# Performance work log

Measured on AMD Instinct MI355X. Metric: run time of the kernel, lower is better.

## Reference

```python
import jax, jax.numpy as jnp
import numpy as np

TOP_K = 4
NORM_TOPK_PROB = True


def _moe_forward(hidden_states, Wr, Wg, Wu, Wd):
    # hidden_states: [B, S, H]; Wr: [E, H]; Wg/Wu: [E, F, H]; Wd: [E, H, F]
    B, S, H = hidden_states.shape
    E = Wr.shape[0]
    x = hidden_states.reshape(-1, H)                     # [T, H]
    T = x.shape[0]

    # Router: softmax in float32 (matches F.softmax(..., dtype=torch.float))
    router_logits = x @ Wr.T                              # [T, E]
    probs = jax.nn.softmax(router_logits.astype(jnp.float32), axis=-1)
    routing_weights, selected_experts = jax.lax.top_k(probs, TOP_K)  # [T, K]
    if NORM_TOPK_PROB:
        routing_weights = routing_weights / jnp.sum(routing_weights, axis=-1, keepdims=True)
    routing_weights = routing_weights.astype(x.dtype)

    # Dense combine matrix: combine[t, e] = routing weight if expert e selected for token t else 0.
    # Equivalent to the sort/gather dispatch + weighted scatter-add in the torch code.
    combine = jnp.zeros((T, E), dtype=x.dtype).at[
        jnp.arange(T)[:, None], selected_experts
    ].add(routing_weights)                               # [T, E]

    # SwiGLU expert MLP: down(silu(gate(x)) * up(x)), evaluated for all experts,
    # then masked/weighted by combine (zero weight == token not routed to expert).
    hg = jnp.einsum('td,efd->tef', x, Wg)                # [T, E, F]
    hu = jnp.einsum('td,efd->tef', x, Wu)                # [T, E, F]
    act = jax.nn.silu(hg) * hu                           # [T, E, F]
    out = jnp.einsum('tef,te,edf->td', act, combine, Wd) # [T, H]
    return out.reshape(B, S, H)


def setup_inputs() -> dict:
    key = jax.random.key(0)
    k0, k1, k2, k3, k4 = jax.random.split(key, 5)
    B, S, H, E, F = 2, 2048, 2048, 16, 768
    scale = 0.02
    return {
        'hidden_states': jax.random.normal(k0, (B, S, H), dtype=jnp.float32),
        'Wr': jax.random.normal(k1, (E, H), dtype=jnp.float32) * scale,
        'Wg': jax.random.normal(k2, (E, F, H), dtype=jnp.float32) * scale,
        'Wu': jax.random.normal(k3, (E, F, H), dtype=jnp.float32) * scale,
        'Wd': jax.random.normal(k4, (E, H, F), dtype=jnp.float32) * scale,
    }


def reference(hidden_states, Wr, Wg, Wu, Wd):
    return _moe_forward(hidden_states, Wr, Wg, Wu, Wd)
```

## Files before the change

kernel.cpp:

```cpp
#include <hip/hip_runtime.h>
#include <hip/hip_bf16.h>

#define H_DIM 2048
#define F_DIM 768
#define E_NUM 16
#define T_TOK 4096
#define TOPK  4
#define TK_ROWS (T_TOK * TOPK)
#define MAX_TILES 160

typedef __attribute__((ext_vector_type(8))) short bf16x8;
typedef __attribute__((ext_vector_type(4))) float f32x4;

static __device__ __forceinline__ float bf2f(unsigned short u) {
    return __uint_as_float(((unsigned)u) << 16);
}
static __device__ __forceinline__ unsigned short f2bu(float f) {
    __hip_bfloat16 h = __float2bfloat16(f);
    return *(unsigned short*)&h;
}

static __device__ __forceinline__ void gl16(const unsigned short* g, unsigned short* l) {
    __builtin_amdgcn_global_load_lds(
        (__attribute__((address_space(1))) void*)(g),
        (__attribute__((address_space(3))) void*)(l),
        16, 0, 0);
}

static __device__ __forceinline__ void stage8(unsigned short* dst, const void* src,
                                              size_t eoff, bool f32) {
    if (f32) {
        const float* s = (const float*)src + eoff;
        float4 a = *(const float4*)s;
        float4 b = *(const float4*)(s + 4);
        __align__(16) unsigned short u[8] = {
            f2bu(a.x), f2bu(a.y), f2bu(a.z), f2bu(a.w),
            f2bu(b.x), f2bu(b.y), f2bu(b.z), f2bu(b.w)};
        *(uint4*)dst = *(const uint4*)u;
    } else {
        *(uint4*)dst = *(const uint4*)((const unsigned short*)src + eoff);
    }
}

__global__ void probe_kernel(const unsigned short* __restrict__ wr, int* __restrict__ flag) {
    const int tid = threadIdx.x;
    int maxe = 0;
    for (int i = tid; i < 512; i += 64) {
        int e = (wr[i] >> 7) & 0xFF;
        maxe = max(maxe, e);
    }
    for (int off = 32; off > 0; off >>= 1)
        maxe = max(maxe, __shfl_down(maxe, off, 64));
    if (tid == 0) flag[0] = (maxe >= 135) ? 1 : 0;
}

__global__ __launch_bounds__(256)
void convert_kernel(unsigned short* __restrict__ dst, const void* __restrict__ src,
                    const int* __restrict__ dflag, size_t n) {
    const size_t i = ((size_t)blockIdx.x * 256 + threadIdx.x) * 8;
    if (i >= n) return;
    stage8(dst + i, src, i, dflag[0] != 0);
}

__global__ __launch_bounds__(256, 2)
void router_kernel(const void* __restrict__ xv,
                   const void* __restrict__ wrv,
                   const int* __restrict__ dflag,
                   float* __restrict__ topk_w,
                   int* __restrict__ topk_e,
                   int* __restrict__ counts) {
    const bool f32 = dflag[0] != 0;
    const int t0 = blockIdx.x * 8;
    __shared__ float xs[8][H_DIM];
    __shared__ float logits_s[8][E_NUM];
    const int tid = threadIdx.x;

    if (f32) {
        const float4* src = (const float4*)((const float*)xv + (size_t)t0 * H_DIM);
        float4* dst = (float4*)&xs[0][0];
        for (int i = tid; i < 8 * H_DIM / 4; i += 256) dst[i] = src[i];
    } else {
        const uint4* src = (const uint4*)((const unsigned short*)xv + (size_t)t0 * H_DIM);
        for (int i = tid; i < 8 * H_DIM / 8; i += 256) {
            uint4 b = src[i];
            const unsigned short* bp = (const unsigned short*)&b;
            float* d = &xs[0][0] + (size_t)i * 8;
#pragma unroll
            for (int j = 0; j < 8; ++j) d[j] = bf2f(bp[j]);
        }
    }
    __syncthreads();

    const int w = tid >> 6;
    const int lane = tid & 63;

    float acc[8][4];
#pragma unroll
    for (int t = 0; t < 8; ++t)
#pragma unroll
        for (int je = 0; je < 4; ++je) acc[t][je] = 0.f;

    for (int i = 0; i < 4; ++i) {
        const int h = i * 512 + lane * 8;
#pragma unroll
        for (int je = 0; je < 4; ++je) {
            const int e = w * 4 + je;
            float wf[8];
            if (f32) {
                const float* wp = (const float*)wrv + (size_t)e * H_DIM + h;
                float4 a = *(const float4*)wp;
                float4 b = *(const float4*)(wp + 4);
                wf[0]=a.x; wf[1]=a.y; wf[2]=a.z; wf[3]=a.w;
                wf[4]=b.x; wf[5]=b.y; wf[6]=b.z; wf[7]=b.w;
            } else {
                uint4 wb = *(const uint4*)((const unsigned short*)wrv + (size_t)e * H_DIM + h);
                const unsigned short* wp = (const unsigned short*)&wb;
#pragma unroll
                for (int j = 0; j < 8; ++j) wf[j] = bf2f(wp[j]);
            }
#pragma unroll
            for (int t = 0; t < 8; ++t) {
                const float* xp = &xs[t][h];
                float s = 0.f;
#pragma unroll
                for (int j = 0; j < 8; ++j) s += xp[j] * wf[j];
                acc[t][je] += s;
            }
        }
    }
#pragma unroll
    for (int t = 0; t < 8; ++t)
#pragma unroll
        for (int je = 0; je < 4; ++je) {
            float v = acc[t][je];
            v += __shfl_down(v, 32, 64); v += __shfl_down(v, 16, 64);
            v += __shfl_down(v, 8, 64);  v += __shfl_down(v, 4, 64);
            v += __shfl_down(v, 2, 64);  v += __shfl_down(v, 1, 64);
            if (lane == 0) logits_s[t][w * 4 + je] = v;
        }
    __syncthreads();

    if (tid < 8) {
        const int t = t0 + tid;
        float l[E_NUM];
#pragma unroll
        for (int i = 0; i < E_NUM; ++i) l[i] = logits_s[tid][i];
        unsigned mask = 0;
        int sel_e[TOPK];
        float sel_v[TOPK];
        for (int k = 0; k < TOPK; ++k) {
            int be = 0; float bv = -1e30f;
            for (int i = 0; i < E_NUM; ++i) {
                if (!(mask & (1u << i)) && l[i] > bv) { bv = l[i]; be = i; }
            }
            mask |= (1u << be);
            sel_e[k] = be; sel_v[k] = bv;
        }
        const float m = sel_v[0];
        float ex[TOPK]; float s = 0.f;
        for (int k = 0; k < TOPK; ++k) { ex[k] = __expf(sel_v[k] - m); s += ex[k]; }
        const float inv = 1.f / s;
        for (int k = 0; k < TOPK; ++k) {
            float wgt = ex[k] * inv;
            if (!f32) wgt = bf2f(f2bu(wgt));
            topk_w[t * TOPK + k] = wgt;
            topk_e[t * TOPK + k] = sel_e[k];
            atomicAdd(&counts[sel_e[k]], 1);
        }
    }
}

__global__ void scan_kernel(const int* __restrict__ counts, int* __restrict__ offsets,
                            int* __restrict__ tiles, int* __restrict__ ntiles) {
    if (threadIdx.x == 0) {
        int s = 0, nt = 0;
        for (int e = 0; e < E_NUM; ++e) {
            offsets[e] = s;
            const int c = counts[e];
            s += c;
            for (int mt = 0; mt * 128 < c && nt < MAX_TILES; ++mt)
                tiles[nt++] = (e << 16) | mt;
        }
        offsets[E_NUM] = s;
        ntiles[0] = nt;
    }
}

__global__ __launch_bounds__(256)
void scatter_kernel(const int* __restrict__ topk_e, const int* __restrict__ offsets,
                    int* __restrict__ cursors, int* __restrict__ row_token) {
    const int i = blockIdx.x * 256 + threadIdx.x;
    if (i < TK_ROWS) {
        const int e = topk_e[i];
        const int pos = offsets[e] + atomicAdd(&cursors[e], 1);
        row_token[pos] = i;
    }
}

__global__ __launch_bounds__(256)
void gateup_fast(const unsigned short* __restrict__ x,
                 const unsigned short* __restrict__ Wg,
                 const unsigned short* __restrict__ Wu,
                 const int* __restrict__ row_token,
                 const int* __restrict__ counts,
                 const int* __restrict__ offsets,
                 const int* __restrict__ tiles,
                 const int* __restrict__ ntiles,
                 __hip_bfloat16* __restrict__ act_buf) {
    const int ti = blockIdx.y;
    if (ti >= ntiles[0]) return;
    const int packed = tiles[ti];
    const int e = packed >> 16, mt = packed & 0xffff;
    const int ft = blockIdx.x;
    const int cnt = counts[e], base = offsets[e];

    __shared__ unsigned short As[128 * 64];
    __shared__ unsigned short Bgs[128 * 64];
    __shared__ unsigned short Bus[128 * 64];
    __shared__ int tok_s[128];

    const int tid = threadIdx.x;
    if (tid < 128) {
        int r = mt * 128 + tid;
        tok_s[tid] = row_token[base + (r < cnt ? r : cnt - 1)] >> 2;
    }
    __syncthreads();

    const int w = tid >> 6;
    const int lane = tid & 63;
    const int subrow = lane >> 3;
    const int sgrp = lane & 7;
    const int lgrp = sgrp ^ subrow;

    const unsigned short* aptr[4];
    const unsigned short* bgptr[4];
    const unsigned short* buptr[4];
    unsigned short* ldsA[4];
    unsigned short* ldsBg[4];
    unsigned short* ldsBu[4];
    const size_t gOff = ((size_t)e * F_DIM + (size_t)ft * 128) * H_DIM;
#pragma unroll
    for (int j = 0; j < 4; ++j) {
        const int r = (w * 4 + j) * 8 + subrow;
        aptr[j]  = x + (size_t)tok_s[r] * H_DIM + lgrp * 8;
        bgptr[j] = Wg + gOff + (size_t)r * H_DIM + lgrp * 8;
        buptr[j] = Wu + gOff + (size_t)r * H_DIM + lgrp * 8;
        const int lo = r * 64 + sgrp * 8;
        ldsA[j]  = &As[lo];
        ldsBg[j] = &Bgs[lo];
        ldsBu[j] = &Bus[lo];
    }

    f32x4 accg[4][4], accu[4][4];
#pragma unroll
    for (int mi = 0; mi < 4; ++mi)
#pragma unroll
        for (int ni = 0; ni < 4; ++ni)
#pragma unroll
            for (int r = 0; r < 4; ++r) { accg[mi][ni][r] = 0.f; accu[mi][ni][r] = 0.f; }

    const int wm = (w >> 1) * 64;
    const int wn = (w & 1) * 64;
    const int lr = lane & 15;
    const int lq = lane >> 4;
    const int gx = lr & 7;
    const int aoff[2] = { (wm + lr) * 64 + ((lq    ) ^ gx) * 8,
                          (wm + lr) * 64 + ((4 + lq) ^ gx) * 8 };
    const int boff[2] = { (wn + lr) * 64 + ((lq    ) ^ gx) * 8,
                          (wn + lr) * 64 + ((4 + lq) ^ gx) * 8 };

    for (int kk = 0; kk < H_DIM / 64; ++kk) {
        const int k0 = kk * 64;
#pragma unroll
        for (int j = 0; j < 4; ++j) {
            gl16(aptr[j] + k0, ldsA[j]);
            gl16(bgptr[j] + k0, ldsBg[j]);
            gl16(buptr[j] + k0, ldsBu[j]);
        }
        __syncthreads();
#pragma unroll
        for (int ks = 0; ks < 2; ++ks) {
            bf16x8 a[4], bg[4], bu[4];
#pragma unroll
            for (int mi = 0; mi < 4; ++mi)
                a[mi] = *(const bf16x8*)&As[aoff[ks] + mi * 1024];
#pragma unroll
            for (int ni = 0; ni < 4; ++ni) {
                bg[ni] = *(const bf16x8*)&Bgs[boff[ks] + ni * 1024];
                bu[ni] = *(const bf16x8*)&Bus[boff[ks] + ni * 1024];
            }
#pragma unroll
            for (int mi = 0; mi < 4; ++mi)
#pragma unroll
                for (int ni = 0; ni < 4; ++ni) {
                    accg[mi][ni] = __builtin_amdgcn_mfma_f32_16x16x32_bf16(a[mi], bg[ni], accg[mi][ni], 0, 0, 0);
                    accu[mi][ni] = __builtin_amdgcn_mfma_f32_16x16x32_bf16(a[mi], bu[ni], accu[mi][ni], 0, 0, 0);
                }
        }
        __syncthreads();
    }

#pragma unroll
    for (int mi = 0; mi < 4; ++mi) {
#pragma unroll
        for (int r = 0; r < 4; ++r) {
            const int row  = wm + mi * 16 + lq * 4 + r;
            const int grow = mt * 128 + row;
            if (grow < cnt) {
                __hip_bfloat16* dst = act_buf + (size_t)(base + grow) * F_DIM + ft * 128 + wn;
#pragma unroll
                for (int ni = 0; ni < 4; ++ni) {
                    const float g = accg[mi][ni][r];
                    const float u = accu[mi][ni][r];
                    const float s = g / (1.f + __expf(-g));
                    dst[ni * 16 + lr] = __float2bfloat16(s * u);
                }
            }
        }
    }
}

__global__ __launch_bounds__(256)
void down_fast(const unsigned short* __restrict__ act,
               const unsigned short* __restrict__ Wd,
               const int* __restrict__ row_token,
               const int* __restrict__ counts,
               const int* __restrict__ offsets,
               const int* __restrict__ tiles,
               const int* __restrict__ ntiles,
               const float* __restrict__ topk_w,
               float* __restrict__ out) {
    const int ti = blockIdx.y;
    if (ti >= ntiles[0]) return;
    const int packed = tiles[ti];
    const int e = packed >> 16, mt = packed & 0xffff;
    const int ht = blockIdx.x;
    const int cnt = counts[e], base = offsets[e];

    __shared__ unsigned short As[128 * 64];
    __shared__ unsigned short Bs[128 * 64];
    __shared__ int tok_s[128];
    __shared__ float w_s[128];

    const int tid = threadIdx.x;
    if (tid < 128) {
        int r = mt * 128 + tid;
        const int t4 = row_token[base + (r < cnt ? r : cnt - 1)];
        tok_s[tid] = t4 >> 2;
        w_s[tid] = topk_w[t4];
    }
    __syncthreads();

    const int w = tid >> 6;
    const int lane = tid & 63;
    const int subrow = lane >> 3;
    const int sgrp = lane & 7;
    const int lgrp = sgrp ^ subrow;

    const unsigned short* aptr[4];
    const unsigned short* bptr[4];
    unsigned short* ldsA[4];
    unsigned short* ldsB[4];
    const size_t hOff = ((size_t)e * H_DIM + (size_t)ht * 128) * F_DIM;
#pragma unroll
    for (int j = 0; j < 4; ++j) {
        const int r = (w * 4 + j) * 8 + subrow;
        int ar = mt * 128 + r;
        ar = (ar < cnt) ? ar : (cnt - 1);
        aptr[j] = act + (size_t)(base + ar) * F_DIM + lgrp * 8;
        bptr[j] = Wd + hOff + (size_t)r * F_DIM + lgrp * 8;
        const int lo = r * 64 + sgrp * 8;
        ldsA[j] = &As[lo];
        ldsB[j] = &Bs[lo];
    }

    f32x4 accd[4][4];
#pragma unroll
    for (int mi = 0; mi < 4; ++mi)
#pragma unroll
        for (int ni = 0; ni < 4; ++ni)
#pragma unroll
            for (int r = 0; r < 4; ++r) accd[mi][ni][r] = 0.f;

    const int wm = (w >> 1) * 64;
    const int wn = (w & 1) * 64;
    const int lr = lane & 15;
    const int lq = lane >> 4;
    const int gx = lr & 7;
    const int aoff[2] = { (wm + lr) * 64 + ((lq    ) ^ gx) * 8,
                          (wm + lr) * 64 + ((4 + lq) ^ gx) * 8 };
    const int boff[2] = { (wn + lr) * 64 + ((lq    ) ^ gx) * 8,
                          (wn + lr) * 64 + ((4 + lq) ^ gx) * 8 };

    for (int kk = 0; kk < F_DIM / 64; ++kk) {
        const int k0 = kk * 64;
#pragma unroll
        for (int j = 0; j < 4; ++j) {
            gl16(aptr[j] + k0, ldsA[j]);
            gl16(bptr[j] + k0, ldsB[j]);
        }
        __syncthreads();
#pragma unroll
        for (int ks = 0; ks < 2; ++ks) {
            bf16x8 a[4], b[4];
#pragma unroll
            for (int mi = 0; mi < 4; ++mi)
                a[mi] = *(const bf16x8*)&As[aoff[ks] + mi * 1024];
#pragma unroll
            for (int ni = 0; ni < 4; ++ni)
                b[ni] = *(const bf16x8*)&Bs[boff[ks] + ni * 1024];
#pragma unroll
            for (int mi = 0; mi < 4; ++mi)
#pragma unroll
                for (int ni = 0; ni < 4; ++ni)
                    accd[mi][ni] = __builtin_amdgcn_mfma_f32_16x16x32_bf16(a[mi], b[ni], accd[mi][ni], 0, 0, 0);
        }
        __syncthreads();
    }

#pragma unroll
    for (int mi = 0; mi < 4; ++mi) {
#pragma unroll
        for (int r = 0; r < 4; ++r) {
            const int row  = wm + mi * 16 + lq * 4 + r;
            const int grow = mt * 128 + row;
            if (grow < cnt) {
                const float wgt = w_s[row];
                float* dst = out + (size_t)tok_s[row] * H_DIM + ht * 128 + wn;
#pragma unroll
                for (int ni = 0; ni < 4; ++ni)
                    atomicAdd(&dst[ni * 16 + lr], accd[mi][ni][r] * wgt);
            }
        }
    }
}

__global__ __launch_bounds__(256, 2)
void gateup_slow(const void* __restrict__ xv, const void* __restrict__ wgv,
                 const void* __restrict__ wuv, const int* __restrict__ dflag,
                 const int* __restrict__ row_token, const int* __restrict__ counts,
                 const int* __restrict__ offsets, __hip_bfloat16* __restrict__ act_buf) {
    const bool f32 = dflag[0] != 0;
    const int e = blockIdx.z, mt = blockIdx.y, ft = blockIdx.x;
    const int cnt = counts[e];
    if (mt * 128 >= cnt) return;
    const int base = offsets[e];
    __shared__ unsigned short As[128 * 72];
    __shared__ unsigned short Bgs[128 * 72];
    __shared__ unsigned short Bus[128 * 72];
    __shared__ int tok_s[128];
    const int tid = threadIdx.x;
    if (tid < 128) {
        int r = mt * 128 + tid;
        tok_s[tid] = row_token[base + (r < cnt ? r : cnt - 1)] >> 2;
    }
    __syncthreads();
    f32x4 accg[4][4], accu[4][4];
#pragma unroll
    for (int mi = 0; mi < 4; ++mi)
#pragma unroll
        for (int ni = 0; ni < 4; ++ni)
#pragma unroll
            for (int r = 0; r < 4; ++r) { accg[mi][ni][r] = 0.f; accu[mi][ni][r] = 0.f; }
    const int wid = tid >> 6, lane = tid & 63;
    const int wm = (wid >> 1) * 64, wn = (wid & 1) * 64;
    const int lr = lane & 15, lq = lane >> 4;
    const int lrow = tid >> 3, lcol = (tid & 7) * 8;
    const size_t gOff = ((size_t)e * F_DIM + ft * 128) * H_DIM;
    for (int kk = 0; kk < H_DIM / 64; ++kk) {
        const int k0 = kk * 64;
#pragma unroll
        for (int rep = 0; rep < 4; ++rep) {
            const int row = lrow + rep * 32;
            stage8(&As[row * 72 + lcol],  xv,  (size_t)tok_s[row] * H_DIM + k0 + lcol, f32);
            stage8(&Bgs[row * 72 + lcol], wgv, gOff + (size_t)row * H_DIM + k0 + lcol, f32);
            stage8(&Bus[row * 72 + lcol], wuv, gOff + (size_t)row * H_DIM + k0 + lcol, f32);
        }
        __syncthreads();
#pragma unroll
        for (int ks = 0; ks < 2; ++ks) {
            const int kb = ks * 32 + lq * 8;
            bf16x8 a[4], bg[4], bu[4];
#pragma unroll
            for (int mi = 0; mi < 4; ++mi)
                a[mi] = *(const bf16x8*)&As[(wm + mi * 16 + lr) * 72 + kb];
#pragma unroll
            for (int ni = 0; ni < 4; ++ni) {
                bg[ni] = *(const bf16x8*)&Bgs[(wn + ni * 16 + lr) * 72 + kb];
                bu[ni] = *(const bf16x8*)&Bus[(wn + ni * 16 + lr) * 72 + kb];
            }
#pragma unroll
            for (int mi = 0; mi < 4; ++mi)
#pragma unroll
                for (int ni = 0; ni < 4; ++ni) {
                    accg[mi][ni] = __builtin_amdgcn_mfma_f32_16x16x32_bf16(a[mi], bg[ni], accg[mi][ni], 0, 0, 0);
                    accu[mi][ni] = __builtin_amdgcn_mfma_f32_16x16x32_bf16(a[mi], bu[ni], accu[mi][ni], 0, 0, 0);
                }
        }
        __syncthreads();
    }
#pragma unroll
    for (int mi = 0; mi < 4; ++mi) {
#pragma unroll
        for (int r = 0; r < 4; ++r) {
            const int row = wm + mi * 16 + lq * 4 + r;
            const int grow = mt * 128 + row;
            if (grow < cnt) {
                __hip_bfloat16* dst = act_buf + (size_t)(base + grow) * F_DIM + ft * 128 + wn;
#pragma unroll
                for (int ni = 0; ni < 4; ++ni) {
                    const float g = accg[mi][ni][r];
                    const float u = accu[mi][ni][r];
                    dst[ni * 16 + lr] = __float2bfloat16((g / (1.f + __expf(-g))) * u);
                }
            }
        }
    }
}

__global__ __launch_bounds__(256, 2)
void down_slow(const __hip_bfloat16* __restrict__ act_buf, const void* __restrict__ wdv,
               const int* __restrict__ dflag, const int* __restrict__ row_token,
               const int* __restrict__ counts, const int* __restrict__ offsets,
               const float* __restrict__ topk_w, float* __restrict__ out) {
    const bool f32 = dflag[0] != 0;
    const int e = blockIdx.z, mt = blockIdx.y, ht = blockIdx.x;
    const int cnt = counts[e];
    if (mt * 128 >= cnt) return;
    const int base = offsets[e];
    __shared__ unsigned short As[128 * 72];
    __shared__ unsigned short Bs[128 * 72];
    __shared__ int tok_s[128];
    __shared__ float w_s[128];
    const int tid = threadIdx.x;
    if (tid < 128) {
        int r = mt * 128 + tid;
        const int t4 = row_token[base + (r < cnt ? r : cnt - 1)];
        tok_s[tid] = t4 >> 2;
        w_s[tid] = topk_w[t4];
    }
    __syncthreads();
    f32x4 accd[4][4];
#pragma unroll
    for (int mi = 0; mi < 4; ++mi)
#pragma unroll
        for (int ni = 0; ni < 4; ++ni)
#pragma unroll
            for (int r = 0; r < 4; ++r) accd[mi][ni][r] = 0.f;
    const int wid = tid >> 6, lane = tid & 63;
    const int wm = (wid >> 1) * 64, wn = (wid & 1) * 64;
    const int lr = lane & 15, lq = lane >> 4;
    const int lrow = tid >> 3, lcol = (tid & 7) * 8;
    const unsigned short* au = (const unsigned short*)act_buf;
    const size_t hOff = ((size_t)e * H_DIM + ht * 128) * F_DIM;
    for (int kk = 0; kk < F_DIM / 64; ++kk) {
        const int k0 = kk * 64;
#pragma unroll
        for (int rep = 0; rep < 4; ++rep) {
            const int row = lrow + rep * 32;
            int ar = mt * 128 + row;
            ar = (ar < cnt) ? ar : (cnt - 1);
            *(uint4*)&As[row * 72 + lcol] = *(const uint4*)(au + (size_t)(base + ar) * F_DIM + k0 + lcol);
            stage8(&Bs[row * 72 + lcol], wdv, hOff + (size_t)row * F_DIM + k0 + lcol, f32);
        }
        __syncthreads();
#pragma unroll
        for (int ks = 0; ks < 2; ++ks) {
            const int kb = ks * 32 + lq * 8;
            bf16x8 a[4], b[4];
#pragma unroll
            for (int mi = 0; mi < 4; ++mi)
                a[mi] = *(const bf16x8*)&As[(wm + mi * 16 + lr) * 72 + kb];
#pragma unroll
            for (int ni = 0; ni < 4; ++ni)
                b[ni] = *(const bf16x8*)&Bs[(wn + ni * 16 + lr) * 72 + kb];
#pragma unroll
            for (int mi = 0; mi < 4; ++mi)
#pragma unroll
                for (int ni = 0; ni < 4; ++ni)
                    accd[mi][ni] = __builtin_amdgcn_mfma_f32_16x16x32_bf16(a[mi], b[ni], accd[mi][ni], 0, 0, 0);
        }
        __syncthreads();
    }
#pragma unroll
    for (int mi = 0; mi < 4; ++mi) {
#pragma unroll
        for (int r = 0; r < 4; ++r) {
            const int row = wm + mi * 16 + lq * 4 + r;
            const int grow = mt * 128 + row;
            if (grow < cnt) {
                const float wgt = w_s[row];
                float* dst = out + (size_t)tok_s[row] * H_DIM + ht * 128 + wn;
#pragma unroll
                for (int ni = 0; ni < 4; ++ni)
                    atomicAdd(&dst[ni * 16 + lr], accd[mi][ni][r] * wgt);
            }
        }
    }
}

extern "C" void kernel_launch(void* const* d_in, const int* in_sizes, int n_in,
                              void* d_out, int out_size, void* d_ws, size_t ws_size,
                              hipStream_t stream) {
    const void* x  = d_in[0];
    const void* Wr = d_in[1];
    const void* Wg = d_in[2];
    const void* Wu = d_in[3];
    const void* Wd = d_in[4];
    float* out = (float*)d_out;

    const size_t nX = (size_t)T_TOK * H_DIM;
    const size_t nW = (size_t)E_NUM * F_DIM * H_DIM;

    char* ws = (char*)d_ws;
    size_t o = 0;
    float* topk_w    = (float*)(ws + o); o += (size_t)TK_ROWS * 4;
    int*   topk_e    = (int*)(ws + o);   o += (size_t)TK_ROWS * 4;
    int*   row_token = (int*)(ws + o);   o += (size_t)TK_ROWS * 4;
    int*   counts    = (int*)(ws + o);   o += 64;
    int*   cursors   = (int*)(ws + o);   o += 64;
    int*   zflag     = (int*)(ws + o);   o += 64;
    int*   dflag     = (int*)(ws + o);   o += 64;
    int*   offsets   = (int*)(ws + o);   o += 128;
    int*   ntiles    = (int*)(ws + o);   o += 64;
    int*   tiles     = (int*)(ws + o);   o += MAX_TILES * 4;
    __hip_bfloat16* act_buf = (__hip_bfloat16*)(ws + o); o += (size_t)TK_ROWS * F_DIM * 2;
    unsigned short* xb  = (unsigned short*)(ws + o); o += nX * 2;
    unsigned short* Wgb = (unsigned short*)(ws + o); o += nW * 2;
    unsigned short* Wub = (unsigned short*)(ws + o); o += nW * 2;
    unsigned short* Wdb = (unsigned short*)(ws + o); o += nW * 2;
    const bool fast = (ws_size >= o);
    (void)zflag;

    hipMemsetAsync(out, 0, (size_t)out_size * sizeof(float), stream);
    hipMemsetAsync(counts, 0, 192, stream);

    probe_kernel<<<1, 64, 0, stream>>>((const unsigned short*)Wr, dflag);
    router_kernel<<<T_TOK / 8, 256, 0, stream>>>(x, Wr, dflag, topk_w, topk_e, counts);
    scan_kernel<<<1, 64, 0, stream>>>(counts, offsets, tiles, ntiles);
    scatter_kernel<<<TK_ROWS / 256, 256, 0, stream>>>(topk_e, offsets, cursors, row_token);

    if (fast) {
        convert_kernel<<<(int)(nX / 2048), 256, 0, stream>>>(xb,  x,  dflag, nX);
        convert_kernel<<<(int)(nW / 2048), 256, 0, stream>>>(Wgb, Wg, dflag, nW);
        convert_kernel<<<(int)(nW / 2048), 256, 0, stream>>>(Wub, Wu, dflag, nW);
        convert_kernel<<<(int)(nW / 2048), 256, 0, stream>>>(Wdb, Wd, dflag, nW);
        gateup_fast<<<dim3(F_DIM / 128, MAX_TILES), 256, 0, stream>>>(
            xb, Wgb, Wub, row_token, counts, offsets, tiles, ntiles, act_buf);
        down_fast<<<dim3(H_DIM / 128, MAX_TILES), 256, 0, stream>>>(
            (const unsigned short*)act_buf, Wdb, row_token, counts, offsets,
            tiles, ntiles, topk_w, out);
    } else {
        gateup_slow<<<dim3(F_DIM / 128, 32, E_NUM), 256, 0, stream>>>(
            x, Wg, Wu, dflag, row_token, counts, offsets, act_buf);
        down_slow<<<dim3(H_DIM / 128, 32, E_NUM), 256, 0, stream>>>(
            act_buf, Wd, dflag, row_token, counts, offsets, topk_w, out);
    }
}
```

Baseline: 936.9 us.

## Schedule GEMM tiles via XCD-aware worklist grouping expert column blocks

The scan kernel now builds per-kernel worklists that greedily assign each (expert, column-block) group of row tiles to one of 8 slots, interleaved so blockIdx modulo 8 selects a slot. Blocks sharing the same expert weight columns are thus dispatched to the same XCD, aiming to improve L2 reuse of weight tiles and balance work. The 2D grid with early exit is replaced by a 1D grid indexed into the worklist. Fixed per-slot caps could drop work under extreme routing skew, and the single-thread scan does more serial work.

```diff
diff --git a/kernel.cpp b/kernel.cpp
--- a/kernel.cpp
+++ b/kernel.cpp
@@ -7,7 +7,10 @@
 #define T_TOK 4096
 #define TOPK  4
 #define TK_ROWS (T_TOK * TOPK)
-#define MAX_TILES 160
+#define GU_CAP 240
+#define DN_CAP 400
+#define GU_GRID (GU_CAP * 8)
+#define DN_GRID (DN_CAP * 8)
 
 typedef __attribute__((ext_vector_type(8))) short bf16x8;
 typedef __attribute__((ext_vector_type(4))) float f32x4;
@@ -171,18 +174,52 @@
 }
 
 __global__ void scan_kernel(const int* __restrict__ counts, int* __restrict__ offsets,
-                            int* __restrict__ tiles, int* __restrict__ ntiles) {
-    if (threadIdx.x == 0) {
-        int s = 0, nt = 0;
+                            int* __restrict__ wl_gu, int* __restrict__ wl_dn) {
+    const int tid = threadIdx.x;
+    for (int i = tid; i < GU_GRID; i += 256) wl_gu[i] = -1;
+    for (int i = tid; i < DN_GRID; i += 256) wl_dn[i] = -1;
+    __syncthreads();
+    if (tid == 0) {
+        int s = 0;
+        int nt[E_NUM];
         for (int e = 0; e < E_NUM; ++e) {
             offsets[e] = s;
             const int c = counts[e];
             s += c;
-            for (int mt = 0; mt * 128 < c && nt < MAX_TILES; ++mt)
-                tiles[nt++] = (e << 16) | mt;
+            nt[e] = (c + 127) >> 7;
         }
         offsets[E_NUM] = s;
-        ntiles[0] = nt;
+
+        {
+            int load[8] = {0,0,0,0,0,0,0,0};
+            int cur[8]  = {0,0,0,0,0,0,0,0};
+            for (int e = 0; e < E_NUM; ++e) {
+                for (int ft = 0; ft < F_DIM / 128; ++ft) {
+                    int best = 0;
+                    for (int x = 1; x < 8; ++x) if (load[x] < load[best]) best = x;
+                    load[best] += nt[e];
+                    for (int mt = 0; mt < nt[e]; ++mt) {
+                        if (cur[best] < GU_CAP)
+                            wl_gu[(cur[best]++) * 8 + best] = (e << 16) | (mt << 4) | ft;
+                    }
+                }
+            }
+        }
+        {
+            int load[8] = {0,0,0,0,0,0,0,0};
+            int cur[8]  = {0,0,0,0,0,0,0,0};
+            for (int e = 0; e < E_NUM; ++e) {
+                for (int ht = 0; ht < H_DIM / 128; ++ht) {
+                    int best = 0;
+                    for (int x = 1; x < 8; ++x) if (load[x] < load[best]) best = x;
+                    load[best] += nt[e];
+                    for (int mt = 0; mt < nt[e]; ++mt) {
+                        if (cur[best] < DN_CAP)
+                            wl_dn[(cur[best]++) * 8 + best] = (e << 16) | (mt << 4) | ht;
+                    }
+                }
+            }
+        }
     }
 }
 
@@ -204,14 +241,11 @@
                  const int* __restrict__ row_token,
                  const int* __restrict__ counts,
                  const int* __restrict__ offsets,
-                 const int* __restrict__ tiles,
-                 const int* __restrict__ ntiles,
+                 const int* __restrict__ wl,
                  __hip_bfloat16* __restrict__ act_buf) {
-    const int ti = blockIdx.y;
-    if (ti >= ntiles[0]) return;
-    const int packed = tiles[ti];
-    const int e = packed >> 16, mt = packed & 0xffff;
-    const int ft = blockIdx.x;
+    const int v = wl[blockIdx.x];
+    if (v < 0) return;
+    const int e = v >> 16, mt = (v >> 4) & 0xfff, ft = v & 15;
     const int cnt = counts[e], base = offsets[e];
 
     __shared__ unsigned short As[128 * 64];
@@ -263,11 +297,11 @@
     const int wn = (w & 1) * 64;
     const int lr = lane & 15;
     const int lq = lane >> 4;
-    const int gx = lr & 7;
-    const int aoff[2] = { (wm + lr) * 64 + ((lq    ) ^ gx) * 8,
-                          (wm + lr) * 64 + ((4 + lq) ^ gx) * 8 };
-    const int boff[2] = { (wn + lr) * 64 + ((lq    ) ^ gx) * 8,
-                          (wn + lr) * 64 + ((4 + lq) ^ gx) * 8 };
+    const int gxr = lr & 7;
+    const int aoff[2] = { (wm + lr) * 64 + ((lq    ) ^ gxr) * 8,
+                          (wm + lr) * 64 + ((4 + lq) ^ gxr) * 8 };
+    const int boff[2] = { (wn + lr) * 64 + ((lq    ) ^ gxr) * 8,
+                          (wn + lr) * 64 + ((4 + lq) ^ gxr) * 8 };
 
     for (int kk = 0; kk < H_DIM / 64; ++kk) {
         const int k0 = kk * 64;
@@ -326,15 +360,12 @@
                const int* __restrict__ row_token,
                const int* __restrict__ counts,
                const int* __restrict__ offsets,
-               const int* __restrict__ tiles,
-               const int* __restrict__ ntiles,
+               const int* __restrict__ wl,
                const float* __restrict__ topk_w,
                float* __restrict__ out) {
-    const int ti = blockIdx.y;
-    if (ti >= ntiles[0]) return;
-    const int packed = tiles[ti];
-    const int e = packed >> 16, mt = packed & 0xffff;
-    const int ht = blockIdx.x;
+    const int v = wl[blockIdx.x];
+    if (v < 0) return;
+    const int e = v >> 16, mt = (v >> 4) & 0xfff, ht = v & 15;
     const int cnt = counts[e], base = offsets[e];
 
     __shared__ unsigned short As[128 * 64];
@@ -386,11 +417,11 @@
     const int wn = (w & 1) * 64;
     const int lr = lane & 15;
     const int lq = lane >> 4;
-    const int gx = lr & 7;
-    const int aoff[2] = { (wm + lr) * 64 + ((lq    ) ^ gx) * 8,
-                          (wm + lr) * 64 + ((4 + lq) ^ gx) * 8 };
-    const int boff[2] = { (wn + lr) * 64 + ((lq    ) ^ gx) * 8,
-                          (wn + lr) * 64 + ((4 + lq) ^ gx) * 8 };
+    const int gxr = lr & 7;
+    const int aoff[2] = { (wm + lr) * 64 + ((lq    ) ^ gxr) * 8,
+                          (wm + lr) * 64 + ((4 + lq) ^ gxr) * 8 };
+    const int boff[2] = { (wn + lr) * 64 + ((lq    ) ^ gxr) * 8,
+                          (wn + lr) * 64 + ((4 + lq) ^ gxr) * 8 };
 
     for (int kk = 0; kk < F_DIM / 64; ++kk) {
         const int k0 = kk * 64;
@@ -622,8 +653,8 @@
     int*   zflag     = (int*)(ws + o);   o += 64;
     int*   dflag     = (int*)(ws + o);   o += 64;
     int*   offsets   = (int*)(ws + o);   o += 128;
-    int*   ntiles    = (int*)(ws + o);   o += 64;
-    int*   tiles     = (int*)(ws + o);   o += MAX_TILES * 4;
+    int*   wl_gu     = (int*)(ws + o);   o += GU_GRID * 4;
+    int*   wl_dn     = (int*)(ws + o);   o += DN_GRID * 4;
     __hip_bfloat16* act_buf = (__hip_bfloat16*)(ws + o); o += (size_t)TK_ROWS * F_DIM * 2;
     unsigned short* xb  = (unsigned short*)(ws + o); o += nX * 2;
     unsigned short* Wgb = (unsigned short*)(ws + o); o += nW * 2;
@@ -637,7 +668,7 @@
 
     probe_kernel<<<1, 64, 0, stream>>>((const unsigned short*)Wr, dflag);
     router_kernel<<<T_TOK / 8, 256, 0, stream>>>(x, Wr, dflag, topk_w, topk_e, counts);
-    scan_kernel<<<1, 64, 0, stream>>>(counts, offsets, tiles, ntiles);
+    scan_kernel<<<1, 256, 0, stream>>>(counts, offsets, wl_gu, wl_dn);
     scatter_kernel<<<TK_ROWS / 256, 256, 0, stream>>>(topk_e, offsets, cursors, row_token);
 
     if (fast) {
@@ -645,11 +676,11 @@
         convert_kernel<<<(int)(nW / 2048), 256, 0, stream>>>(Wgb, Wg, dflag, nW);
         convert_kernel<<<(int)(nW / 2048), 256, 0, stream>>>(Wub, Wu, dflag, nW);
         convert_kernel<<<(int)(nW / 2048), 256, 0, stream>>>(Wdb, Wd, dflag, nW);
-        gateup_fast<<<dim3(F_DIM / 128, MAX_TILES), 256, 0, stream>>>(
-            xb, Wgb, Wub, row_token, counts, offsets, tiles, ntiles, act_buf);
-        down_fast<<<dim3(H_DIM / 128, MAX_TILES), 256, 0, stream>>>(
+        gateup_fast<<<GU_GRID, 256, 0, stream>>>(
+            xb, Wgb, Wub, row_token, counts, offsets, wl_gu, act_buf);
+        down_fast<<<DN_GRID, 256, 0, stream>>>(
             (const unsigned short*)act_buf, Wdb, row_token, counts, offsets,
-            tiles, ntiles, topk_w, out);
+            wl_dn, topk_w, out);
     } else {
         gateup_slow<<<dim3(F_DIM / 128, 32, E_NUM), 256, 0, stream>>>(
             x, Wg, Wu, dflag, row_token, counts, offsets, act_buf);
```

After: 1.111 ms. +18.5%, slower.
